# Optimization experiments

Hardware: AMD Instinct MI355X
Metric: run time of the kernel (lower is better)

## Reference

```python
import jax, jax.numpy as jnp
import numpy as np
from jax.ops import segment_sum

N_NODES = 100000
N_EDGES = 1600000
N_LABEL = 200000
IN_C, HID_C, OUT_C = 128, 128, 64


def setup_inputs() -> dict:
    key = jax.random.key(0)
    ks = jax.random.split(key, 6)
    x = jax.random.normal(ks[0], (N_NODES, IN_C), dtype=jnp.float32)
    edge_index = jax.random.randint(ks[1], (2, N_EDGES), 0, N_NODES, dtype=jnp.int64)
    edge_label_index = jax.random.randint(ks[2], (2, N_LABEL), 0, N_NODES, dtype=jnp.int64)
    W1 = jax.random.normal(ks[3], (IN_C, HID_C), dtype=jnp.float32) / np.sqrt(IN_C)
    b1 = jnp.zeros((HID_C,), dtype=jnp.float32)
    W2 = jax.random.normal(ks[4], (HID_C, OUT_C), dtype=jnp.float32) / np.sqrt(HID_C)
    b2 = jnp.zeros((OUT_C,), dtype=jnp.float32)
    return {"x": x, "edge_index": edge_index, "edge_label_index": edge_label_index,
            "W1": W1, "b1": b1, "W2": W2, "b2": b2}


def gcn_conv(x, W, b, src, dst, num_nodes):
    # PyG GCNConv: linear transform, add self-loops, symmetric normalization, sum-aggregate, bias.
    h = x @ W                                            # [N, C_out]
    loop = jnp.arange(num_nodes, dtype=src.dtype)
    s = jnp.concatenate([src, loop])                     # [E + N]
    d = jnp.concatenate([dst, loop])
    deg = segment_sum(jnp.ones_like(d, dtype=h.dtype), d, num_segments=num_nodes)
    dinv = jnp.where(deg > 0, jax.lax.rsqrt(deg), 0.0)   # deg^-1/2
    norm = dinv[s] * dinv[d]                             # [E + N]
    msg = h[s] * norm[:, None]                           # gather + scale
    out = segment_sum(msg, d, num_segments=num_nodes)    # scatter-add aggregate
    return out + b


def reference(x, edge_index, edge_label_index, W1, b1, W2, b2):
    src, dst = edge_index[0], edge_index[1]
    n = x.shape[0]
    h = jax.nn.relu(gcn_conv(x, W1, b1, src, dst, n))
    z = gcn_conv(h, W2, b2, src, dst, n)                 # encode
    # decode: dot product over candidate edges
    return jnp.sum(z[edge_label_index[0]] * z[edge_label_index[1]], axis=-1)
```

## Files before the change

### kernel.cpp

```cpp
#include <hip/hip_runtime.h>

typedef __attribute__((ext_vector_type(8))) short bfrag8;
typedef __attribute__((ext_vector_type(4))) float facc4;

__device__ __forceinline__ unsigned int f2bf(float f) {
    unsigned int u = __float_as_uint(f);
    return (u + 0x7FFFu + ((u >> 16) & 1u)) >> 16;
}
__device__ __forceinline__ float bf_lo(unsigned int w) { return __uint_as_float(w << 16); }
__device__ __forceinline__ float bf_hi(unsigned int w) { return __uint_as_float(w & 0xffff0000u); }


#define CNT_B 2048

__global__ void k_prep(const float* __restrict__ x, const float* __restrict__ W1,
                       const float* __restrict__ W2, unsigned short* __restrict__ x16,
                       unsigned short* __restrict__ w1t, unsigned short* __restrict__ w2t,
                       const int* __restrict__ dst, int* __restrict__ cnt,
                       unsigned int* __restrict__ pack, int e, int nx8) {
    int b = blockIdx.x;
    if (b < CNT_B) {
        for (int i = b * 256 + threadIdx.x; i < e; i += CNT_B * 256) {
            int d = dst[i];
            int r = atomicAdd(&cnt[d], 1);
            pack[i] = ((unsigned int)d << 14) | (unsigned int)r;
        }
        return;
    }
    int t = (b - CNT_B) * 256 + threadIdx.x;
    if (t < nx8) {
        const float4* xp = reinterpret_cast<const float4*>(x) + (long)t * 2;
        float4 a = xp[0], v = xp[1];
        uint4 o;
        o.x = f2bf(a.x) | (f2bf(a.y) << 16);
        o.y = f2bf(a.z) | (f2bf(a.w) << 16);
        o.z = f2bf(v.x) | (f2bf(v.y) << 16);
        o.w = f2bf(v.z) | (f2bf(v.w) << 16);
        reinterpret_cast<uint4*>(x16)[t] = o;
    } else {
        int u = t - nx8;
        if (u < 128 * 128) {
            int k = u >> 7, nn = u & 127;
            w1t[nn * 128 + k] = (unsigned short)f2bf(W1[u]);
        } else if ((u -= 128 * 128) < 128 * 64) {
            int k = u >> 6, nn = u & 63;
            w2t[nn * 128 + k] = (unsigned short)f2bf(W2[u]);
        }
    }
}

#define SCP 1024

__global__ void k_scan_a(const int* __restrict__ cnt, int* __restrict__ part, int n) {
    int p = blockIdx.x * blockDim.x + threadIdx.x;
    if (p >= SCP) return;
    int chunk = (n + SCP - 1) / SCP;
    int b = p * chunk, e = min(b + chunk, n), s = 0;
    for (int i = b; i < e; ++i) s += cnt[i];
    part[p] = s;
}

__global__ void k_scan_b(int* __restrict__ part) {
    __shared__ int sm[SCP];
    int t = threadIdx.x;
    sm[t] = part[t];
    __syncthreads();
    for (int off = 1; off < SCP; off <<= 1) {
        int v = (t >= off) ? sm[t - off] : 0;
        __syncthreads();
        sm[t] += v;
        __syncthreads();
    }
    part[t] = t ? sm[t - 1] : 0;
}

__global__ void k_scan_c(const int* __restrict__ cnt, const int* __restrict__ part,
                         int* __restrict__ rowptr, float* __restrict__ dinv, int n) {
    int p = blockIdx.x * blockDim.x + threadIdx.x;
    if (p >= SCP) return;
    int chunk = (n + SCP - 1) / SCP;
    int b = p * chunk, e = min(b + chunk, n);
    int run = part[p];
    for (int i = b; i < e; ++i) {
        rowptr[i] = run;
        dinv[i] = rsqrtf((float)(cnt[i] + 1));
        run += cnt[i];
    }
    if (p == SCP - 1) rowptr[n] = run;
}


#define FILL_G 192

__device__ __forceinline__ void fill_role(const int* __restrict__ src,
                                          const unsigned int* __restrict__ pack,
                                          const int* __restrict__ rowptr,
                                          int* __restrict__ csr_src,
                                          int e, float scale, int r, int g) {
    int chunk = (e + FILL_G - 1) / FILL_G;
    int beg = g * chunk, end = min(beg + chunk, e);
    for (int i = beg + threadIdx.x; i < end; i += blockDim.x) {
        unsigned int p = pack[i];
        int d = (int)(p >> 14);
        if ((int)((float)d * scale) == r) {
            int pos = rowptr[d] + (int)(p & 0x3FFFu);
            csr_src[pos] = src[i];
        }
    }
}


__global__ __launch_bounds__(256) void k_fuse(
        const int* __restrict__ src, const unsigned int* __restrict__ pack,
        const int* __restrict__ rowptr, int* __restrict__ csr_src, int e, float scale,
        const unsigned short* __restrict__ X16, const unsigned short* __restrict__ W1T,
        const float* __restrict__ dinv, unsigned short* __restrict__ H16, int n) {
    __shared__ unsigned short sA[128 * 64];
    __shared__ unsigned short sB[128 * 64];

    int t8 = blockIdx.x >> 3, l8 = blockIdx.x & 7;
    int m = t8 % 3, q = t8 / 3;

    if (m < 2) {
        int g = q * 2 + m;
        if (g < FILL_G)
            fill_role(src, pack, rowptr, csr_src, e, scale, l8, g);
        return;
    }

    int bid = q * 8 + l8;
    int row0 = bid * 128;
    if (row0 >= n) return;

    int tid = threadIdx.x;
    int lane = tid & 63;
    int wv = tid >> 6;

    facc4 acc[2][8];
#pragma unroll
    for (int i = 0; i < 2; ++i)
#pragma unroll
        for (int j = 0; j < 8; ++j) acc[i][j] = (facc4)0.f;

    for (int s = 0; s < 2; ++s) {
        if (s) __syncthreads();
#pragma unroll
        for (int it = 0; it < 4; ++it) {
            int chunk = it * 4 + wv;
            int L = chunk * 64 + lane;
            int row = L >> 3, gp = L & 7;
            int gsrc = gp ^ (row & 7);
            int grow = min(row0 + row, n - 1);
            const unsigned short* srcp = X16 + (long)grow * 128 + s * 64 + gsrc * 8;
            unsigned short* dstp = sA + chunk * 512;
            __builtin_amdgcn_global_load_lds(
                (const __attribute__((address_space(1))) void*)srcp,
                (__attribute__((address_space(3))) void*)dstp, 16, 0, 0);
        }
#pragma unroll
        for (int it = 0; it < 4; ++it) {
            int chunk = it * 4 + wv;
            int L = chunk * 64 + lane;
            int row = L >> 3, gp = L & 7;
            int gsrc = gp ^ (row & 7);
            const unsigned short* srcp = W1T + (long)row * 128 + s * 64 + gsrc * 8;
            unsigned short* dstp = sB + chunk * 512;
            __builtin_amdgcn_global_load_lds(
                (const __attribute__((address_space(1))) void*)srcp,
                (__attribute__((address_space(3))) void*)dstp, 16, 0, 0);
        }
        __syncthreads();

        bfrag8 af[2][2];
#pragma unroll
        for (int mt = 0; mt < 2; ++mt)
#pragma unroll
            for (int ks = 0; ks < 2; ++ks) {
                int r = wv * 32 + mt * 16 + (lane & 15);
                int g = ks * 4 + (lane >> 4);
                af[mt][ks] = *reinterpret_cast<const bfrag8*>(&sA[r * 64 + (g ^ (r & 7)) * 8]);
            }
#pragma unroll
        for (int nt = 0; nt < 8; ++nt) {
            int nr = nt * 16 + (lane & 15);
            bfrag8 b0 = *reinterpret_cast<const bfrag8*>(&sB[nr * 64 + (((lane >> 4)) ^ (nr & 7)) * 8]);
            bfrag8 b1 = *reinterpret_cast<const bfrag8*>(&sB[nr * 64 + ((4 + (lane >> 4)) ^ (nr & 7)) * 8]);
            acc[0][nt] = __builtin_amdgcn_mfma_f32_16x16x32_bf16(af[0][0], b0, acc[0][nt], 0, 0, 0);
            acc[1][nt] = __builtin_amdgcn_mfma_f32_16x16x32_bf16(af[1][0], b0, acc[1][nt], 0, 0, 0);
            acc[0][nt] = __builtin_amdgcn_mfma_f32_16x16x32_bf16(af[0][1], b1, acc[0][nt], 0, 0, 0);
            acc[1][nt] = __builtin_amdgcn_mfma_f32_16x16x32_bf16(af[1][1], b1, acc[1][nt], 0, 0, 0);
        }
    }

#pragma unroll
    for (int mt = 0; mt < 2; ++mt)
#pragma unroll
        for (int reg = 0; reg < 4; ++reg) {
            int r = row0 + wv * 32 + mt * 16 + (lane >> 4) * 4 + reg;
            if (r < n) {
                float dv = dinv[r];
#pragma unroll
                for (int nt = 0; nt < 8; ++nt)
                    H16[(long)r * 128 + nt * 16 + (lane & 15)] =
                        (unsigned short)f2bf(acc[mt][nt][reg] * dv);
            }
        }
}


__global__ __launch_bounds__(256) void k_gemmM64(const unsigned short* __restrict__ H16,
                                                 const unsigned short* __restrict__ W2T,
                                                 const float* __restrict__ dinv,
                                                 unsigned short* __restrict__ Z16, int n) {
    __shared__ unsigned short sA[128 * 64];
    __shared__ unsigned short sB[64 * 64];

    int row0 = blockIdx.x * 128;
    int tid = threadIdx.x;
    int lane = tid & 63;
    int wv = tid >> 6;

    facc4 acc[2][4];
#pragma unroll
    for (int i = 0; i < 2; ++i)
#pragma unroll
        for (int j = 0; j < 4; ++j) acc[i][j] = (facc4)0.f;

    for (int s = 0; s < 2; ++s) {
        if (s) __syncthreads();
#pragma unroll
        for (int it = 0; it < 4; ++it) {
            int chunk = it * 4 + wv;
            int L = chunk * 64 + lane;
            int row = L >> 3, gp = L & 7;
            int gsrc = gp ^ (row & 7);
            int grow = min(row0 + row, n - 1);
            const unsigned short* srcp = H16 + (long)grow * 128 + s * 64 + gsrc * 8;
            unsigned short* dstp = sA + chunk * 512;
            __builtin_amdgcn_global_load_lds(
                (const __attribute__((address_space(1))) void*)srcp,
                (__attribute__((address_space(3))) void*)dstp, 16, 0, 0);
        }
#pragma unroll
        for (int it = 0; it < 2; ++it) {
            int chunk = it * 4 + wv;
            int L = chunk * 64 + lane;
            int row = L >> 3, gp = L & 7;
            int gsrc = gp ^ (row & 7);
            const unsigned short* srcp = W2T + (long)row * 128 + s * 64 + gsrc * 8;
            unsigned short* dstp = sB + chunk * 512;
            __builtin_amdgcn_global_load_lds(
                (const __attribute__((address_space(1))) void*)srcp,
                (__attribute__((address_space(3))) void*)dstp, 16, 0, 0);
        }
        __syncthreads();

        bfrag8 af[2][2];
#pragma unroll
        for (int mt = 0; mt < 2; ++mt)
#pragma unroll
            for (int ks = 0; ks < 2; ++ks) {
                int r = wv * 32 + mt * 16 + (lane & 15);
                int g = ks * 4 + (lane >> 4);
                af[mt][ks] = *reinterpret_cast<const bfrag8*>(&sA[r * 64 + (g ^ (r & 7)) * 8]);
            }
#pragma unroll
        for (int nt = 0; nt < 4; ++nt) {
            int nr = nt * 16 + (lane & 15);
            bfrag8 b0 = *reinterpret_cast<const bfrag8*>(&sB[nr * 64 + (((lane >> 4)) ^ (nr & 7)) * 8]);
            bfrag8 b1 = *reinterpret_cast<const bfrag8*>(&sB[nr * 64 + ((4 + (lane >> 4)) ^ (nr & 7)) * 8]);
            acc[0][nt] = __builtin_amdgcn_mfma_f32_16x16x32_bf16(af[0][0], b0, acc[0][nt], 0, 0, 0);
            acc[1][nt] = __builtin_amdgcn_mfma_f32_16x16x32_bf16(af[1][0], b0, acc[1][nt], 0, 0, 0);
            acc[0][nt] = __builtin_amdgcn_mfma_f32_16x16x32_bf16(af[0][1], b1, acc[0][nt], 0, 0, 0);
            acc[1][nt] = __builtin_amdgcn_mfma_f32_16x16x32_bf16(af[1][1], b1, acc[1][nt], 0, 0, 0);
        }
    }

#pragma unroll
    for (int mt = 0; mt < 2; ++mt)
#pragma unroll
        for (int reg = 0; reg < 4; ++reg) {
            int r = row0 + wv * 32 + mt * 16 + (lane >> 4) * 4 + reg;
            if (r < n) {
                float dv = dinv[r];
#pragma unroll
                for (int nt = 0; nt < 4; ++nt)
                    Z16[(long)r * 64 + nt * 16 + (lane & 15)] =
                        (unsigned short)f2bf(acc[mt][nt][reg] * dv);
            }
        }
}


template<int C, bool RELU, bool OB>
__global__ void k_gather16(const int* __restrict__ rowptr, const int* __restrict__ csr_src,
                           const float* __restrict__ dinv, const unsigned short* __restrict__ h16,
                           const float* __restrict__ bias, void* __restrict__ outv, int n) {
    const int TPN = C / 8;
    const int RS = C / 8;
    int t = blockIdx.x * blockDim.x + threadIdx.x;
    int node = t / TPN;
    if (node >= n) return;
    int cg = t % TPN;

    const uint4* h4 = reinterpret_cast<const uint4*>(h16);
    float acc[8];
    {
        uint4 u = h4[(long)node * RS + cg];
        acc[0] = bf_lo(u.x); acc[1] = bf_hi(u.x);
        acc[2] = bf_lo(u.y); acc[3] = bf_hi(u.y);
        acc[4] = bf_lo(u.z); acc[5] = bf_hi(u.z);
        acc[6] = bf_lo(u.w); acc[7] = bf_hi(u.w);
    }

    int beg = rowptr[node], end = rowptr[node + 1];
    int e = beg;
    for (; e + 8 <= end; e += 8) {
        int s[8];
#pragma unroll
        for (int q = 0; q < 8; ++q) s[q] = csr_src[e + q];
        uint4 u[8];
#pragma unroll
        for (int q = 0; q < 8; ++q) u[q] = h4[(long)s[q] * RS + cg];
#pragma unroll
        for (int q = 0; q < 8; ++q) {
            acc[0] += bf_lo(u[q].x); acc[1] += bf_hi(u[q].x);
            acc[2] += bf_lo(u[q].y); acc[3] += bf_hi(u[q].y);
            acc[4] += bf_lo(u[q].z); acc[5] += bf_hi(u[q].z);
            acc[6] += bf_lo(u[q].w); acc[7] += bf_hi(u[q].w);
        }
    }
    for (; e < end; ++e) {
        uint4 u = h4[(long)csr_src[e] * RS + cg];
        acc[0] += bf_lo(u.x); acc[1] += bf_hi(u.x);
        acc[2] += bf_lo(u.y); acc[3] += bf_hi(u.y);
        acc[4] += bf_lo(u.z); acc[5] += bf_hi(u.z);
        acc[6] += bf_lo(u.w); acc[7] += bf_hi(u.w);
    }

    float dd = dinv[node];
    int c0 = cg * 8;
    float4 ba = *reinterpret_cast<const float4*>(bias + c0);
    float4 bb = *reinterpret_cast<const float4*>(bias + c0 + 4);
    float o[8];
    o[0] = fmaf(acc[0], dd, ba.x); o[1] = fmaf(acc[1], dd, ba.y);
    o[2] = fmaf(acc[2], dd, ba.z); o[3] = fmaf(acc[3], dd, ba.w);
    o[4] = fmaf(acc[4], dd, bb.x); o[5] = fmaf(acc[5], dd, bb.y);
    o[6] = fmaf(acc[6], dd, bb.z); o[7] = fmaf(acc[7], dd, bb.w);
    if (RELU) {
#pragma unroll
        for (int i = 0; i < 8; ++i) o[i] = fmaxf(o[i], 0.f);
    }
    if (OB) {
        uint4 w;
        w.x = f2bf(o[0]) | (f2bf(o[1]) << 16);
        w.y = f2bf(o[2]) | (f2bf(o[3]) << 16);
        w.z = f2bf(o[4]) | (f2bf(o[5]) << 16);
        w.w = f2bf(o[6]) | (f2bf(o[7]) << 16);
        *reinterpret_cast<uint4*>((unsigned short*)outv + (long)node * C + c0) = w;
    } else {
        float* of = (float*)outv + (long)node * C + c0;
        *reinterpret_cast<float4*>(of) = make_float4(o[0], o[1], o[2], o[3]);
        *reinterpret_cast<float4*>(of + 4) = make_float4(o[4], o[5], o[6], o[7]);
    }
}


__global__ void k_decode16(const int* __restrict__ ia, const int* __restrict__ ib,
                           const unsigned short* __restrict__ z, float* __restrict__ out, int m) {
    int t = blockIdx.x * blockDim.x + threadIdx.x;
    int k = t >> 3;
    if (k >= m) return;
    int cg = t & 7;
    int a = ia[k], b = ib[k];
    const uint4* z4 = reinterpret_cast<const uint4*>(z);
    uint4 ua = z4[(long)a * 8 + cg];
    uint4 ub = z4[(long)b * 8 + cg];
    float dot = bf_lo(ua.x) * bf_lo(ub.x) + bf_hi(ua.x) * bf_hi(ub.x)
              + bf_lo(ua.y) * bf_lo(ub.y) + bf_hi(ua.y) * bf_hi(ub.y)
              + bf_lo(ua.z) * bf_lo(ub.z) + bf_hi(ua.z) * bf_hi(ub.z)
              + bf_lo(ua.w) * bf_lo(ub.w) + bf_hi(ua.w) * bf_hi(ub.w);
    dot += __shfl_xor(dot, 4);
    dot += __shfl_xor(dot, 2);
    dot += __shfl_xor(dot, 1);
    if (cg == 0) out[k] = dot;
}


extern "C" void kernel_launch(void* const* d_in, const int* in_sizes, int n_in,
                              void* d_out, int out_size, void* d_ws, size_t ws_size,
                              hipStream_t stream) {
    const float* x  = (const float*)d_in[0];
    const int*   ei = (const int*)d_in[1];
    const int*   el = (const int*)d_in[2];
    const float* W1 = (const float*)d_in[3];
    const float* b1 = (const float*)d_in[4];
    const float* W2 = (const float*)d_in[5];
    const float* b2 = (const float*)d_in[6];
    float* out = (float*)d_out;

    const int N = in_sizes[0] / 128;
    const int E = in_sizes[1] / 2;
    const int L = out_size;

    const int* src = ei;
    const int* dst = ei + E;
    const int* la  = el;
    const int* lb  = el + L;

    char* wsb = (char*)d_ws;

    unsigned short* ht16 = (unsigned short*)wsb;
    unsigned short* zt16 = (unsigned short*)wsb;
    unsigned short* z16  = (unsigned short*)(wsb + (size_t)N * 256);

    unsigned int*   pack = (unsigned int*)(wsb + (size_t)N * 512);
    unsigned short* h16  = (unsigned short*)(wsb + (size_t)N * 512);
    unsigned short* x16  = (unsigned short*)(wsb + (size_t)N * 512 + (size_t)N * 256);

    int*   csr_src = (int*)(wsb + (size_t)N * 1024);
    int*   cnt     = csr_src + E;
    int*   rowptr  = cnt + N;
    float* dinv    = (float*)(rowptr + N + 1);
    int*   part    = (int*)(dinv + N);
    unsigned short* w1t = (unsigned short*)(part + SCP);
    unsigned short* w2t = w1t + 128 * 128;

    auto cdiv = [](long a, long b) { return (int)((a + b - 1) / b); };

    hipMemsetAsync(cnt, 0, (size_t)N * sizeof(int), stream);
    int nx8 = N * 16;
    int cvtB = cdiv((long)nx8 + 128 * 128 + 128 * 64, 256);
    k_prep<<<CNT_B + cvtB, 256, 0, stream>>>(x, W1, W2, x16, w1t, w2t,
                                             dst, cnt, pack, E, nx8);

    k_scan_a<<<SCP / 256, 256, 0, stream>>>(cnt, part, N);
    k_scan_b<<<1, SCP, 0, stream>>>(part);
    k_scan_c<<<SCP / 256, 256, 0, stream>>>(cnt, part, rowptr, dinv, N);

    k_fuse<<<294 * 8, 256, 0, stream>>>(src, pack, rowptr, csr_src, E, 8.0f / (float)N,
                                        x16, w1t, dinv, ht16, N);

    k_gather16<128, true, true><<<cdiv((long)N * 16, 256), 256, 0, stream>>>(
        rowptr, csr_src, dinv, ht16, b1, h16, N);

    k_gemmM64<<<cdiv(N, 128), 256, 0, stream>>>(h16, w2t, dinv, zt16, N);
    k_gather16<64, false, true><<<cdiv((long)N * 8, 256), 256, 0, stream>>>(
        rowptr, csr_src, dinv, zt16, b2, z16, N);

    k_decode16<<<cdiv((long)L * 8, 256), 256, 0, stream>>>(la, lb, z16, out, L);
}
```

Baseline: 318.9 us.

## Fuse layer-1 gather aggregation with layer-2 GEMM in one kernel

```diff
diff --git a/kernel.cpp b/kernel.cpp
--- a/kernel.cpp
+++ b/kernel.cpp
@@ -109,7 +109,6 @@
     }
 }
 
-
 __global__ __launch_bounds__(256) void k_fuse(
         const int* __restrict__ src, const unsigned int* __restrict__ pack,
         const int* __restrict__ rowptr, int* __restrict__ csr_src, int e, float scale,
@@ -208,87 +207,107 @@
 }
 
 
-__global__ __launch_bounds__(256) void k_gemmM64(const unsigned short* __restrict__ H16,
-                                                 const unsigned short* __restrict__ W2T,
-                                                 const float* __restrict__ dinv,
-                                                 unsigned short* __restrict__ Z16, int n) {
-    __shared__ unsigned short sA[128 * 64];
-    __shared__ unsigned short sB[64 * 64];
-
-    int row0 = blockIdx.x * 128;
+__global__ __launch_bounds__(256) void k_gafu(
+        const int* __restrict__ rowptr, const int* __restrict__ csr_src,
+        const float* __restrict__ dinv, const unsigned short* __restrict__ ht16,
+        const float* __restrict__ bias, const unsigned short* __restrict__ W2T,
+        unsigned short* __restrict__ Z16, int n) {
+    __shared__ unsigned short sW2[64 * 128];
+    __shared__ unsigned short sH[16 * 136];
+
     int tid = threadIdx.x;
     int lane = tid & 63;
     int wv = tid >> 6;
 
-    facc4 acc[2][4];
-#pragma unroll
-    for (int i = 0; i < 2; ++i)
-#pragma unroll
-        for (int j = 0; j < 4; ++j) acc[i][j] = (facc4)0.f;
-
-    for (int s = 0; s < 2; ++s) {
-        if (s) __syncthreads();
-#pragma unroll
-        for (int it = 0; it < 4; ++it) {
-            int chunk = it * 4 + wv;
-            int L = chunk * 64 + lane;
-            int row = L >> 3, gp = L & 7;
-            int gsrc = gp ^ (row & 7);
-            int grow = min(row0 + row, n - 1);
-            const unsigned short* srcp = H16 + (long)grow * 128 + s * 64 + gsrc * 8;
-            unsigned short* dstp = sA + chunk * 512;
-            __builtin_amdgcn_global_load_lds(
-                (const __attribute__((address_space(1))) void*)srcp,
-                (__attribute__((address_space(3))) void*)dstp, 16, 0, 0);
-        }
-#pragma unroll
-        for (int it = 0; it < 2; ++it) {
-            int chunk = it * 4 + wv;
-            int L = chunk * 64 + lane;
-            int row = L >> 3, gp = L & 7;
-            int gsrc = gp ^ (row & 7);
-            const unsigned short* srcp = W2T + (long)row * 128 + s * 64 + gsrc * 8;
-            unsigned short* dstp = sB + chunk * 512;
-            __builtin_amdgcn_global_load_lds(
-                (const __attribute__((address_space(1))) void*)srcp,
-                (__attribute__((address_space(3))) void*)dstp, 16, 0, 0);
-        }
-        __syncthreads();
-
-        bfrag8 af[2][2];
-#pragma unroll
-        for (int mt = 0; mt < 2; ++mt)
-#pragma unroll
-            for (int ks = 0; ks < 2; ++ks) {
-                int r = wv * 32 + mt * 16 + (lane & 15);
-                int g = ks * 4 + (lane >> 4);
-                af[mt][ks] = *reinterpret_cast<const bfrag8*>(&sA[r * 64 + (g ^ (r & 7)) * 8]);
+#pragma unroll
+    for (int it = 0; it < 4; ++it) {
+        int L = it * 256 + tid;
+        int row = L >> 4, gp = L & 15;
+        int gsrc = gp ^ (row & 7);
+        const unsigned short* srcp = W2T + (long)row * 128 + gsrc * 8;
+        unsigned short* dstp = sW2 + L * 8;
+        __builtin_amdgcn_global_load_lds(
+            (const __attribute__((address_space(1))) void*)srcp,
+            (__attribute__((address_space(3))) void*)dstp, 16, 0, 0);
+    }
+
+    int node = blockIdx.x * 16 + (tid >> 4);
+    int cg = tid & 15;
+    bool alive = node < n;
+
+    uint4 w = make_uint4(0, 0, 0, 0);
+    if (alive) {
+        const uint4* h4 = reinterpret_cast<const uint4*>(ht16);
+        float acc[8];
+        {
+            uint4 u = h4[(long)node * 16 + cg];
+            acc[0] = bf_lo(u.x); acc[1] = bf_hi(u.x);
+            acc[2] = bf_lo(u.y); acc[3] = bf_hi(u.y);
+            acc[4] = bf_lo(u.z); acc[5] = bf_hi(u.z);
+            acc[6] = bf_lo(u.w); acc[7] = bf_hi(u.w);
+        }
+        int beg = rowptr[node], end = rowptr[node + 1];
+        int e = beg;
+        for (; e + 8 <= end; e += 8) {
+            int s[8];
+#pragma unroll
+            for (int q = 0; q < 8; ++q) s[q] = csr_src[e + q];
+            uint4 u[8];
+#pragma unroll
+            for (int q = 0; q < 8; ++q) u[q] = h4[(long)s[q] * 16 + cg];
+#pragma unroll
+            for (int q = 0; q < 8; ++q) {
+                acc[0] += bf_lo(u[q].x); acc[1] += bf_hi(u[q].x);
+                acc[2] += bf_lo(u[q].y); acc[3] += bf_hi(u[q].y);
+                acc[4] += bf_lo(u[q].z); acc[5] += bf_hi(u[q].z);
+                acc[6] += bf_lo(u[q].w); acc[7] += bf_hi(u[q].w);
             }
-#pragma unroll
-        for (int nt = 0; nt < 4; ++nt) {
-            int nr = nt * 16 + (lane & 15);
-            bfrag8 b0 = *reinterpret_cast<const bfrag8*>(&sB[nr * 64 + (((lane >> 4)) ^ (nr & 7)) * 8]);
-            bfrag8 b1 = *reinterpret_cast<const bfrag8*>(&sB[nr * 64 + ((4 + (lane >> 4)) ^ (nr & 7)) * 8]);
-            acc[0][nt] = __builtin_amdgcn_mfma_f32_16x16x32_bf16(af[0][0], b0, acc[0][nt], 0, 0, 0);
-            acc[1][nt] = __builtin_amdgcn_mfma_f32_16x16x32_bf16(af[1][0], b0, acc[1][nt], 0, 0, 0);
-            acc[0][nt] = __builtin_amdgcn_mfma_f32_16x16x32_bf16(af[0][1], b1, acc[0][nt], 0, 0, 0);
-            acc[1][nt] = __builtin_amdgcn_mfma_f32_16x16x32_bf16(af[1][1], b1, acc[1][nt], 0, 0, 0);
-        }
-    }
-
-#pragma unroll
-    for (int mt = 0; mt < 2; ++mt)
-#pragma unroll
-        for (int reg = 0; reg < 4; ++reg) {
-            int r = row0 + wv * 32 + mt * 16 + (lane >> 4) * 4 + reg;
-            if (r < n) {
-                float dv = dinv[r];
-#pragma unroll
-                for (int nt = 0; nt < 4; ++nt)
-                    Z16[(long)r * 64 + nt * 16 + (lane & 15)] =
-                        (unsigned short)f2bf(acc[mt][nt][reg] * dv);
-            }
-        }
+        }
+        for (; e < end; ++e) {
+            uint4 u = h4[(long)csr_src[e] * 16 + cg];
+            acc[0] += bf_lo(u.x); acc[1] += bf_hi(u.x);
+            acc[2] += bf_lo(u.y); acc[3] += bf_hi(u.y);
+            acc[4] += bf_lo(u.z); acc[5] += bf_hi(u.z);
+            acc[6] += bf_lo(u.w); acc[7] += bf_hi(u.w);
+        }
+        float dd = dinv[node];
+        int c0 = cg * 8;
+        float4 ba = *reinterpret_cast<const float4*>(bias + c0);
+        float4 bb = *reinterpret_cast<const float4*>(bias + c0 + 4);
+        float o[8];
+        o[0] = fmaf(acc[0], dd, ba.x); o[1] = fmaf(acc[1], dd, ba.y);
+        o[2] = fmaf(acc[2], dd, ba.z); o[3] = fmaf(acc[3], dd, ba.w);
+        o[4] = fmaf(acc[4], dd, bb.x); o[5] = fmaf(acc[5], dd, bb.y);
+        o[6] = fmaf(acc[6], dd, bb.z); o[7] = fmaf(acc[7], dd, bb.w);
+#pragma unroll
+        for (int i = 0; i < 8; ++i) o[i] = fmaxf(o[i], 0.f);
+        w.x = f2bf(o[0]) | (f2bf(o[1]) << 16);
+        w.y = f2bf(o[2]) | (f2bf(o[3]) << 16);
+        w.z = f2bf(o[4]) | (f2bf(o[5]) << 16);
+        w.w = f2bf(o[6]) | (f2bf(o[7]) << 16);
+    }
+    *reinterpret_cast<uint4*>(&sH[(tid >> 4) * 136 + cg * 8]) = w;
+    __syncthreads();
+
+    facc4 zacc = (facc4)0.f;
+#pragma unroll
+    for (int ks = 0; ks < 4; ++ks) {
+        bfrag8 a = *reinterpret_cast<const bfrag8*>(
+            &sH[(lane & 15) * 136 + ks * 32 + (lane >> 4) * 8]);
+        int nr = wv * 16 + (lane & 15);
+        int g = ks * 4 + (lane >> 4);
+        bfrag8 b = *reinterpret_cast<const bfrag8*>(&sW2[nr * 128 + (g ^ (nr & 7)) * 8]);
+        zacc = __builtin_amdgcn_mfma_f32_16x16x32_bf16(a, b, zacc, 0, 0, 0);
+    }
+#pragma unroll
+    for (int reg = 0; reg < 4; ++reg) {
+        int r = blockIdx.x * 16 + (lane >> 4) * 4 + reg;
+        if (r < n) {
+            float dv = dinv[r];
+            Z16[(long)r * 64 + wv * 16 + (lane & 15)] =
+                (unsigned short)f2bf(zacc[reg] * dv);
+        }
+    }
 }
 
 
@@ -411,11 +430,10 @@
     char* wsb = (char*)d_ws;
 
     unsigned short* ht16 = (unsigned short*)wsb;
-    unsigned short* zt16 = (unsigned short*)wsb;
     unsigned short* z16  = (unsigned short*)(wsb + (size_t)N * 256);
 
     unsigned int*   pack = (unsigned int*)(wsb + (size_t)N * 512);
-    unsigned short* h16  = (unsigned short*)(wsb + (size_t)N * 512);
+    unsigned short* zt16 = (unsigned short*)(wsb + (size_t)N * 512);
     unsigned short* x16  = (unsigned short*)(wsb + (size_t)N * 512 + (size_t)N * 256);
 
     int*   csr_src = (int*)(wsb + (size_t)N * 1024);
@@ -441,10 +459,8 @@
     k_fuse<<<294 * 8, 256, 0, stream>>>(src, pack, rowptr, csr_src, E, 8.0f / (float)N,
                                         x16, w1t, dinv, ht16, N);
 
-    k_gather16<128, true, true><<<cdiv((long)N * 16, 256), 256, 0, stream>>>(
-        rowptr, csr_src, dinv, ht16, b1, h16, N);
-
-    k_gemmM64<<<cdiv(N, 128), 256, 0, stream>>>(h16, w2t, dinv, zt16, N);
+    k_gafu<<<cdiv(N, 16), 256, 0, stream>>>(rowptr, csr_src, dinv, ht16, b1, w2t, zt16, N);
+
     k_gather16<64, false, true><<<cdiv((long)N * 8, 256), 256, 0, stream>>>(
         rowptr, csr_src, dinv, zt16, b2, z16, N);
 
```

Measured after the change: 313.1 us. About the same (-1.8%).
